# Performance work log

Measured on AMD Instinct MI355X. Metric: run time of the kernel, lower is better.

The kernel has to match this reference:

```python
import jax, jax.numpy as jnp
import numpy as np
import math

B, T, D = 4, 1024, 512
H, HD = 8, 64
FF = 2048
L = 2
MEM = 512
S = T + MEM  # src length
EPS = 1e-5


def _sinusoid(positions, dim):
    pos = positions.astype(jnp.float32)[:, None]                      # [P,1]
    div = jnp.exp(jnp.arange(0, dim, 2, dtype=jnp.float32) * (-math.log(10000.0) / dim))
    enc = jnp.zeros((positions.shape[0], dim), jnp.float32)
    enc = enc.at[:, 0::2].set(jnp.sin(pos * div))
    enc = enc.at[:, 1::2].set(jnp.cos(pos * div))
    return enc


def _layer_norm(x, scale, bias):
    m = jnp.mean(x, axis=-1, keepdims=True)
    v = jnp.var(x, axis=-1, keepdims=True)
    return (x - m) / jnp.sqrt(v + EPS) * scale + bias


def _rel_shift(x):
    # x: [T, S, B, H] -> Transformer-XL relative shift
    t, s, b, h = x.shape
    xp = jnp.concatenate([jnp.zeros((t, 1, b, h), x.dtype), x], axis=1)  # [T,S+1,B,H]
    xp = xp.reshape(s + 1, t, b, h)
    return xp[1:].reshape(t, s, b, h)


def setup_inputs() -> dict:
    key = jax.random.key(0)
    ks = jax.random.split(key, 16)
    w = 0.02
    inp = {
        "x": jax.random.normal(ks[0], (B, T, D), jnp.float32),
        "positions": jnp.arange(S - 1, -1, -1, dtype=jnp.int64 if jax.config.jax_enable_x64 else jnp.int32),
        # causal-with-memory mask: query i (src position i+MEM) cannot see src j > i + MEM
        "attn_mask": jnp.arange(S)[None, :] > (jnp.arange(T)[:, None] + MEM),
        "mems": jax.random.normal(ks[1], (L + 1, MEM, B, D), jnp.float32) * 0.5,
        "u_bias": jax.random.normal(ks[2], (H, HD), jnp.float32) * w,
        "v_bias": jax.random.normal(ks[3], (H, HD), jnp.float32) * w,
        "qkv_w": jax.random.normal(ks[4], (L, 3 * H * HD, D), jnp.float32) * w,
        "pos_w": jax.random.normal(ks[5], (L, H * HD, D), jnp.float32) * w,
        "out_w": jax.random.normal(ks[6], (L, D, H * HD), jnp.float32) * w,
        "lin1_w": jax.random.normal(ks[7], (L, FF, D), jnp.float32) * w,
        "lin1_b": jnp.zeros((L, FF), jnp.float32),
        "lin2_w": jax.random.normal(ks[8], (L, D, FF), jnp.float32) * w,
        "lin2_b": jnp.zeros((L, D), jnp.float32),
        "ln1_s": jnp.ones((L, D), jnp.float32),
        "ln1_b": jnp.zeros((L, D), jnp.float32),
        "ln2_s": jnp.ones((L, D), jnp.float32),
        "ln2_b": jnp.zeros((L, D), jnp.float32),
    }
    return inp


def reference(x, positions, attn_mask, mems, u_bias, v_bias, qkv_w, pos_w, out_w,
              lin1_w, lin1_b, lin2_w, lin2_b, ln1_s, ln1_b, ln2_s, ln2_b):
    scale = 1.0 / math.sqrt(D)  # source uses 1/sqrt(embed_dim)
    xs = jnp.swapaxes(x, 0, 1)                       # [T,B,D] (batch_first -> time-first)
    pe = _sinusoid(positions, D)                     # [S,D]
    out = xs
    hiddens = [xs]
    for l in range(L):
        cat = jnp.concatenate([mems[l], out], axis=0)            # [S,B,D]
        qkv = jnp.einsum('sbd,ed->sbe', cat, qkv_w[l])           # [S,B,3*H*HD]
        q, k, v = jnp.split(qkv, 3, axis=-1)
        q = q[-T:].reshape(T, B, H, HD)
        k = k.reshape(S, B, H, HD)
        v = v.reshape(S, B, H, HD)
        r = jnp.einsum('sd,ed->se', pe, pos_w[l]).reshape(S, H, HD)
        content = jnp.einsum('ibnd,jbnd->ijbn', q + u_bias, k)   # [T,S,B,H]
        pos_sc = jnp.einsum('ibnd,jnd->ijbn', q + v_bias, r)     # [T,S,B,H]
        score = (content + _rel_shift(pos_sc)) * scale
        score = jnp.where(attn_mask[:, :, None, None], -jnp.inf, score)
        attn = jax.nn.softmax(score, axis=1)
        ctx = jnp.einsum('ijbn,jbnd->ibnd', attn, v).reshape(T, B, H * HD)
        a_out = jnp.einsum('tbe,de->tbd', ctx, out_w[l])
        h = _layer_norm(out + a_out, ln1_s[l], ln1_b[l])
        ff = jnp.einsum('tbf,df->tbd', jax.nn.relu(jnp.einsum('tbd,fd->tbf', h, lin1_w[l]) + lin1_b[l]), lin2_w[l]) + lin2_b[l]
        out = _layer_norm(h + ff, ln2_s[l], ln2_b[l])
        hiddens.append(out)
    final = jnp.swapaxes(out[-T:], 0, 1)             # [B,T,D]
    new_mems = jax.lax.stop_gradient(jnp.stack(
        [jnp.concatenate([mems[i], hiddens[i]], axis=0)[-MEM:] for i in range(L + 1)], axis=0))
    return final, new_mems
```

## Files before the change

### kernel.cpp

```cpp
#include <hip/hip_runtime.h>

constexpr int BB = 4, TT = 1024, DD = 512, HH = 8, HDIM = 64;
constexpr int FFD = 2048, NLAYER = 2, MM = 512, SS = 1536;
constexpr float LN_EPS = 1e-5f;
constexpr float SCALE = 0.04419417382415922f;

typedef unsigned short u16;
typedef __attribute__((ext_vector_type(8))) short bf16x8;
typedef __attribute__((ext_vector_type(4))) float f32x4;

__device__ __forceinline__ float b2f(u16 u) {
  union { unsigned int i; float f; } c; c.i = ((unsigned int)u) << 16; return c.f;
}
__device__ __forceinline__ u16 f2b(float f) {
  unsigned int x = __builtin_bit_cast(unsigned int, f);
  x += 0x7fffu + ((x >> 16) & 1u);
  return (u16)(x >> 16);
}

__device__ __forceinline__ void dma16(const u16* g, u16* l) {
  __builtin_amdgcn_global_load_lds(
      (const __attribute__((address_space(1))) unsigned int*)g,
      (__attribute__((address_space(3))) unsigned int*)l, 16, 0, 0);
}

constexpr int OFF_X    = 0;
constexpr int OFF_MEMS = 2097152;
constexpr int OFF_UB   = 5242880;
constexpr int OFF_VB   = 5243392;
constexpr int OFF_QKVW = 5243904;
constexpr int OFF_POSW = 6816768;
constexpr int OFF_OUTW = 7341056;
constexpr int OFF_L1W  = 7865344;
constexpr int OFF_L1B  = 9962496;
constexpr int OFF_L2W  = 9966592;
constexpr int OFF_L2B  = 12063744;
constexpr int OFF_LN1S = 12064768;
constexpr int OFF_LN1B = 12065792;
constexpr int OFF_LN2S = 12066816;
constexpr int OFF_LN2B = 12067840;
constexpr int TOT_IN   = 12068864;

__global__ void txl_probe(const u16* __restrict__ xr, int* __restrict__ flag) {
  int lane = threadIdx.x;
  int cnt = 0;
  for (int k = 0; k < 8; ++k) {
    u16 u = xr[lane * 8 + k];
    int e = (u >> 7) & 0xFF;
    if (e >= 0xC0) ++cnt;
  }
  for (int o = 32; o; o >>= 1) cnt += __shfl_xor(cnt, o);
  if (lane == 0) *flag = (cnt >= 32) ? 1 : 0;
}

__global__ __launch_bounds__(256) void txl_convert(
    const void* x, const void* mems, const void* ub, const void* vb,
    const void* qkvw, const void* posw, const void* outw,
    const void* l1w, const void* l1b, const void* l2w, const void* l2b,
    const void* ln1s, const void* ln1b, const void* ln2s, const void* ln2b,
    u16* __restrict__ dst, const int* __restrict__ flag) {
  int idx = blockIdx.x * 256 + threadIdx.x;
  if (idx >= TOT_IN) return;
  const void* p; int local;
  if      (idx < OFF_MEMS) { p = x;    local = idx; }
  else if (idx < OFF_UB)   { p = mems; local = idx - OFF_MEMS; }
  else if (idx < OFF_VB)   { p = ub;   local = idx - OFF_UB; }
  else if (idx < OFF_QKVW) { p = vb;   local = idx - OFF_VB; }
  else if (idx < OFF_POSW) { p = qkvw; local = idx - OFF_QKVW; }
  else if (idx < OFF_OUTW) { p = posw; local = idx - OFF_POSW; }
  else if (idx < OFF_L1W)  { p = outw; local = idx - OFF_OUTW; }
  else if (idx < OFF_L1B)  { p = l1w;  local = idx - OFF_L1W; }
  else if (idx < OFF_L2W)  { p = l1b;  local = idx - OFF_L1B; }
  else if (idx < OFF_L2B)  { p = l2w;  local = idx - OFF_L2W; }
  else if (idx < OFF_LN1S) { p = l2b;  local = idx - OFF_L2B; }
  else if (idx < OFF_LN1B) { p = ln1s; local = idx - OFF_LN1S; }
  else if (idx < OFF_LN2S) { p = ln1b; local = idx - OFF_LN1B; }
  else if (idx < OFF_LN2B) { p = ln2s; local = idx - OFF_LN2S; }
  else                     { p = ln2b; local = idx - OFF_LN2B; }
  dst[idx] = (*flag) ? f2b(((const float*)p)[local]) : ((const u16*)p)[local];
}

template <int EPI>
__global__ __launch_bounds__(256) void txl_gemm4(const u16* __restrict__ A,
                                                 const u16* __restrict__ B,
                                                 float* __restrict__ C,
                                                 u16* __restrict__ Obf,
                                                 const u16* __restrict__ bias,
                                                 int M, int N, int K, int KS) {
  __shared__ __align__(16) u16 As[2][128 * 32];
  __shared__ __align__(16) u16 Bs[2][128 * 32];
  const int tid = threadIdx.x;
  const int wave = tid >> 6, lane = tid & 63;
  const int wm = (wave & 1) * 64, wn = (wave >> 1) * 64;
  const int m0 = blockIdx.x * 128, n0 = blockIdx.y * 128;
  const int kbeg = blockIdx.z * KS, kend = kbeg + KS;
  const int L15 = lane & 15, quad = lane >> 4;

  auto stage = [&](int k0, int buf) {
    for (int c = 0; c < 2; ++c) {
      int segBase = c * 256 + wave * 64;
      int seg = segBase + lane;
      int row = seg >> 2, q = seg & 3;
      dma16(&A[(size_t)(m0 + row) * K + k0 + q * 8], &As[buf][segBase * 8]);
      dma16(&B[(size_t)(n0 + row) * K + k0 + q * 8], &Bs[buf][segBase * 8]);
    }
  };

  f32x4 acc[4][4] = {};
  stage(kbeg, 0);
  __syncthreads();
  int buf = 0;
  for (int k0 = kbeg; k0 < kend; k0 += 32) {
    if (k0 + 32 < kend) stage(k0 + 32, buf ^ 1);
    bf16x8 af[4], bfr[4];
    for (int t = 0; t < 4; ++t)
      af[t] = *reinterpret_cast<const bf16x8*>(&As[buf][(wm + t * 16 + L15) * 32 + quad * 8]);
    for (int t = 0; t < 4; ++t)
      bfr[t] = *reinterpret_cast<const bf16x8*>(&Bs[buf][(wn + t * 16 + L15) * 32 + quad * 8]);
    for (int tm = 0; tm < 4; ++tm)
      for (int tn = 0; tn < 4; ++tn)
        acc[tm][tn] = __builtin_amdgcn_mfma_f32_16x16x32_bf16(af[tm], bfr[tn], acc[tm][tn], 0, 0, 0);
    buf ^= 1;
    __syncthreads();
  }
  float* Cz = C + (size_t)blockIdx.z * ((size_t)M * N);
  for (int tm = 0; tm < 4; ++tm)
    for (int tn = 0; tn < 4; ++tn) {
      int col = n0 + wn + tn * 16 + L15;
      for (int r = 0; r < 4; ++r) {
        int row = m0 + wm + tm * 16 + quad * 4 + r;
        if (EPI == 0) {
          Cz[(size_t)row * N + col] = acc[tm][tn][r];
        } else {
          float v = acc[tm][tn][r] + b2f(bias[col]);
          Obf[(size_t)row * N + col] = f2b(fmaxf(v, 0.f));
        }
      }
    }
}

__global__ void txl_pe(u16* __restrict__ pe) {
  int idx = blockIdx.x * 256 + threadIdx.x;
  if (idx >= SS * 256) return;
  int p = idx >> 8, m = idx & 255;
  float posf = (float)(SS - 1 - p);
  float div = expf((float)(2 * m) * (-9.210340371976184f / 512.0f));
  float a = posf * div;
  pe[(size_t)p * DD + 2 * m] = f2b(sinf(a));
  pe[(size_t)p * DD + 2 * m + 1] = f2b(cosf(a));
}

__global__ void txl_transpose_in(const u16* __restrict__ x, u16* __restrict__ cur_bf,
                                 float* __restrict__ cur_f, void* __restrict__ outv,
                                 const int* __restrict__ flag) {
  int idx = blockIdx.x * 256 + threadIdx.x;
  if (idx >= BB * TT * DD) return;
  int b = idx >> 19, t = (idx >> 9) & 1023, d = idx & 511;
  u16 v = x[idx];
  size_t o = ((size_t)t * BB + b) * DD + d;
  cur_bf[o] = v; cur_f[o] = b2f(v);
  if (t >= 512) {
    size_t mo = 2097152 + (o - 1048576);
    if (*flag) ((float*)outv)[mo] = b2f(v);
    else       ((u16*)outv)[mo] = v;
  }
}

__global__ void txl_store_final(const u16* __restrict__ cur_bf, void* __restrict__ outv,
                                const int* __restrict__ flag) {
  int idx = blockIdx.x * 256 + threadIdx.x;
  if (idx >= BB * TT * DD) return;
  int b = idx >> 19, t = (idx >> 9) & 1023, d = idx & 511;
  u16 v = cur_bf[((size_t)t * BB + b) * DD + d];
  if (*flag) ((float*)outv)[idx] = b2f(v);
  else       ((u16*)outv)[idx] = v;
}

__global__ __launch_bounds__(256) void txl_qkv_scatter(
    const float* __restrict__ C, const u16* __restrict__ ub, const u16* __restrict__ vb,
    u16* __restrict__ qu, u16* __restrict__ qv, u16* __restrict__ kb) {
  size_t idx = (size_t)blockIdx.x * 256 + threadIdx.x;
  if (idx >= (size_t)SS * BB * 1536) return;
  int e = (int)(idx % 1536);
  if (e >= 1024) return;
  int row = (int)(idx / 1536);
  int s = row >> 2, b = row & 3;
  float val = C[idx];
  if (e < 512) {
    if (s >= MM) {
      int i = s - MM, n = e >> 6, d = e & 63;
      size_t o = ((size_t)(b * HH + n) * TT + i) * HDIM + d;
      qu[o] = f2b(val + b2f(ub[e]));
      qv[o] = f2b(val + b2f(vb[e]));
    }
  } else {
    int e2 = e - 512, n = e2 >> 6, d = e2 & 63;
    kb[((size_t)(b * HH + n) * SS + s) * HDIM + d] = f2b(val);
  }
}

__global__ __launch_bounds__(256) void txl_v_transpose(const float* __restrict__ C,
                                                       u16* __restrict__ vT) {
  __shared__ u16 t[64][68];
  int bx = blockIdx.x;
  int sb = bx >> 5;
  int bn = bx & 31;
  int n = bn & 7, b = bn >> 3;
  int tid = threadIdx.x;
  int s0 = sb * 64;
  {
    int d = tid & 63, sr = tid >> 6;
    for (int i = 0; i < 16; ++i) {
      int s = s0 + sr + i * 4;
      t[sr + i * 4][d] = f2b(C[(size_t)(s * 4 + b) * 1536 + 1024 + n * 64 + d]);
    }
  }
  __syncthreads();
  {
    int s = tid & 63, dr = tid >> 6;
    u16* dst = vT + (size_t)(b * HH + n) * HDIM * SS;
    for (int i = 0; i < 16; ++i) {
      int d2 = dr + i * 4;
      dst[(size_t)d2 * SS + s0 + s] = t[s][d2];
    }
  }
}

__global__ void txl_r_scatter(const float* __restrict__ C, u16* __restrict__ rb) {
  int idx = blockIdx.x * 256 + threadIdx.x;
  if (idx >= SS * DD) return;
  int p = idx >> 9, e = idx & 511;
  int n = e >> 6, d = e & 63;
  rb[((size_t)n * SS + p) * HDIM + d] = f2b(C[idx]);
}

__global__ __launch_bounds__(256) void txl_attn9(
    const u16* __restrict__ qu, const u16* __restrict__ qv, const u16* __restrict__ kbuf,
    const u16* __restrict__ vT, const u16* __restrict__ rbuf,
    float* __restrict__ O0, float* __restrict__ O1,
    float* __restrict__ L0, float* __restrict__ L1) {
  __shared__ __align__(16) u16 Kb[2][2048];
  __shared__ __align__(16) u16 Vb[2][2048];
  __shared__ __align__(16) u16 Rr[8][1024];
  __shared__ __align__(16) u16 ps4[4][640];

  const int bx = blockIdx.x;
  const int n = bx & 7;
  const int rest = bx >> 3;
  const int b = rest & 3;
  const int rest2 = rest >> 2;
  const int st = rest2 & 15;
  const int piece = rest2 >> 4;
  const int i0b = st * 64;
  const int g0 = 63 - (i0b >> 4);
  const int jcEnd = 18 + 2 * st;
  const int half = 9 + st;
  const int jcBeg = piece ? half : 0;
  const int jcLim = piece ? jcEnd : half;
  const int gB = g0 + 2 * jcBeg;

  const int tid = threadIdx.x, w = tid >> 6, lane = tid & 63;
  const int L15 = lane & 15, quad = lane >> 4;
  const int i0w = i0b + 16 * w;
  const int bh = b * HH + n;

  const u16* kB = kbuf + (size_t)bh * SS * HDIM;
  const u16* rB = rbuf + (size_t)n * SS * HDIM;
  const u16* vB = vT + (size_t)bh * HDIM * SS;

  const u16* quB = qu + ((size_t)bh * TT + i0w) * HDIM;
  const u16* qvB = qv + ((size_t)bh * TT + i0w) * HDIM;
  bf16x8 aqu[2], aqv[2];
  for (int c = 0; c < 2; ++c) {
    aqu[c] = *reinterpret_cast<const bf16x8*>(&quB[(size_t)L15 * HDIM + c * 32 + quad * 8]);
    aqv[c] = *reinterpret_cast<const bf16x8*>(&qvB[(size_t)L15 * HDIM + c * 32 + quad * 8]);
  }

  u16* ps = &ps4[w][0];

  auto stageK = [&](int jc) {
    const u16* src = kB + (size_t)(jc * 32 + (lane & 31)) * HDIM + (2 * w + (lane >> 5)) * 8;
    dma16(src, &Kb[jc & 1][512 * w]);
  };
  auto stageV = [&](int jc) {
    const u16* src = vB + (size_t)lane * SS + jc * 32 + 8 * w;
    dma16(src, &Vb[jc & 1][512 * w]);
  };
  auto stageRslab = [&](int slab) {
    int rrow = slab * 16 + (lane & 15);
    rrow = (rrow > SS - 1) ? (SS - 1) : rrow;
    const u16* s0 = rB + (size_t)rrow * HDIM + (lane >> 4) * 8;
    dma16(s0, &Rr[slab & 7][0]);
    dma16(s0 + 32, &Rr[slab & 7][512]);
  };
  auto rfrag = [&](int slab, int h) {
    return *reinterpret_cast<const bf16x8*>(&Rr[slab & 7][((quad + 4 * h) * 16 + L15) * 8]);
  };

  stageK(jcBeg); stageV(jcBeg);
  stageRslab(gB - 3 + w);
  if (w < 2) stageRslab(gB + 1 + w);
  __syncthreads();

  f32x4 pT0 = {};
  pT0 = __builtin_amdgcn_mfma_f32_16x16x32_bf16(aqv[0], rfrag(gB - w, 0), pT0, 0, 0, 0);
  pT0 = __builtin_amdgcn_mfma_f32_16x16x32_bf16(aqv[1], rfrag(gB - w, 1), pT0, 0, 0, 0);

  float l_lane[4] = {0.f, 0.f, 0.f, 0.f};
  f32x4 Oacc[4] = {};

  for (int jc = jcBeg; jc < jcLim; ++jc) {
    if (jc + 1 < jcLim) {
      stageK(jc + 1); stageV(jc + 1);
      if (w < 2) stageRslab(g0 + 3 + 2 * jc + w);
    }
    const int hslot = jc & 1, j0 = jc * 32;
    bf16x8 k00 = *reinterpret_cast<const bf16x8*>(&Kb[hslot][((quad) * 32 + L15) * 8]);
    bf16x8 k01 = *reinterpret_cast<const bf16x8*>(&Kb[hslot][((quad + 4) * 32 + L15) * 8]);
    bf16x8 k10 = *reinterpret_cast<const bf16x8*>(&Kb[hslot][((quad) * 32 + 16 + L15) * 8]);
    bf16x8 k11 = *reinterpret_cast<const bf16x8*>(&Kb[hslot][((quad + 4) * 32 + 16 + L15) * 8]);
    f32x4 s0v = {}, s1v = {};
    s0v = __builtin_amdgcn_mfma_f32_16x16x32_bf16(aqu[0], k00, s0v, 0, 0, 0);
    s0v = __builtin_amdgcn_mfma_f32_16x16x32_bf16(aqu[1], k01, s0v, 0, 0, 0);
    s1v = __builtin_amdgcn_mfma_f32_16x16x32_bf16(aqu[0], k10, s1v, 0, 0, 0);
    s1v = __builtin_amdgcn_mfma_f32_16x16x32_bf16(aqu[1], k11, s1v, 0, 0, 0);
    const int sl1 = g0 - w + 2 * jc + 1;
    f32x4 pT1 = {}, pT2 = {};
    pT1 = __builtin_amdgcn_mfma_f32_16x16x32_bf16(aqv[0], rfrag(sl1, 0), pT1, 0, 0, 0);
    pT1 = __builtin_amdgcn_mfma_f32_16x16x32_bf16(aqv[1], rfrag(sl1, 1), pT1, 0, 0, 0);
    pT2 = __builtin_amdgcn_mfma_f32_16x16x32_bf16(aqv[0], rfrag(sl1 + 1, 0), pT2, 0, 0, 0);
    pT2 = __builtin_amdgcn_mfma_f32_16x16x32_bf16(aqv[1], rfrag(sl1 + 1, 1), pT2, 0, 0, 0);
    for (int r = 0; r < 4; ++r) {
      int ii = quad * 4 + r;
      int i = i0w + ii;
      int c = 15 + L15 - ii;
      int srcLane = (quad << 4) | (c & 15);
      float a0 = __shfl(pT0[r], srcLane);
      float a1 = __shfl(pT1[r], srcLane);
      float b1v = __shfl(pT2[r], srcLane);
      float sv0 = s0v[r] + ((c < 16) ? a0 : a1);
      float sv1 = s1v[r] + ((c < 16) ? a1 : b1v);
      sv0 = (j0 + L15 <= i + MM) ? sv0 : -3e38f;
      sv1 = (j0 + 16 + L15 <= i + MM) ? sv1 : -3e38f;
      float e0 = __expf(sv0 * SCALE);
      float e1 = __expf(sv1 * SCALE);
      l_lane[r] += e0 + e1;
      int row = ii * 40;
      ps[row + L15] = f2b(e0);
      ps[row + 16 + L15] = f2b(e1);
    }
    bf16x8 ap = *reinterpret_cast<const bf16x8*>(&ps[L15 * 40 + quad * 8]);
    bf16x8 v0 = *reinterpret_cast<const bf16x8*>(&Vb[hslot][(quad * 64 + L15) * 8]);
    bf16x8 v1 = *reinterpret_cast<const bf16x8*>(&Vb[hslot][(quad * 64 + 16 + L15) * 8]);
    bf16x8 v2 = *reinterpret_cast<const bf16x8*>(&Vb[hslot][(quad * 64 + 32 + L15) * 8]);
    bf16x8 v3 = *reinterpret_cast<const bf16x8*>(&Vb[hslot][(quad * 64 + 48 + L15) * 8]);
    Oacc[0] = __builtin_amdgcn_mfma_f32_16x16x32_bf16(ap, v0, Oacc[0], 0, 0, 0);
    Oacc[1] = __builtin_amdgcn_mfma_f32_16x16x32_bf16(ap, v1, Oacc[1], 0, 0, 0);
    Oacc[2] = __builtin_amdgcn_mfma_f32_16x16x32_bf16(ap, v2, Oacc[2], 0, 0, 0);
    Oacc[3] = __builtin_amdgcn_mfma_f32_16x16x32_bf16(ap, v3, Oacc[3], 0, 0, 0);
    pT0 = pT2;
    __syncthreads();
  }

  float lsum[4];
  for (int r = 0; r < 4; ++r) {
    float s = l_lane[r];
    for (int o = 1; o < 16; o <<= 1) s += __shfl_xor(s, o);
    lsum[r] = s;
  }
  float* Op = piece ? O1 : O0;
  float* Lp = piece ? L1 : L0;
  for (int tn = 0; tn < 4; ++tn)
    for (int r = 0; r < 4; ++r) {
      int ii = quad * 4 + r;
      Op[((size_t)(i0w + ii) * BB + b) * DD + n * HDIM + tn * 16 + L15] = Oacc[tn][r];
    }
  if (L15 == 0)
    for (int r = 0; r < 4; ++r)
      Lp[(size_t)bh * TT + i0w + quad * 4 + r] = lsum[r];
}

__global__ void txl_attn_merge(const float* __restrict__ O0, const float* __restrict__ O1,
                               const float* __restrict__ L0, const float* __restrict__ L1,
                               u16* __restrict__ ctx) {
  int o = blockIdx.x * 256 + threadIdx.x;
  if (o >= BB * TT * DD) return;
  int i = o >> 11, b = (o >> 9) & 3, e = o & 511, n = e >> 6;
  size_t li = (size_t)(b * HH + n) * TT + i;
  float l = L0[li] + L1[li];
  ctx[o] = f2b((O0[o] + O1[o]) / l);
}

__global__ __launch_bounds__(256) void txl_ln(
    const float* __restrict__ gout, int nparts, const u16* __restrict__ bias,
    const float* __restrict__ resid, const u16* __restrict__ gam, const u16* __restrict__ bet,
    u16* __restrict__ ybf, float* __restrict__ yf,
    void* __restrict__ outv, int off, const int* __restrict__ flag) {
  const int row = blockIdx.x, tid = threadIdx.x;
  const int lane = tid & 63, wave = tid >> 6;
  __shared__ float red[4];
  size_t base = (size_t)row * DD;
  float x0 = resid[base + tid];
  float x1 = resid[base + tid + 256];
  for (int p = 0; p < nparts; ++p) {
    x0 += gout[(size_t)p * 2097152 + base + tid];
    x1 += gout[(size_t)p * 2097152 + base + tid + 256];
  }
  if (bias) { x0 += b2f(bias[tid]); x1 += b2f(bias[tid + 256]); }
  float s = x0 + x1;
  for (int o = 32; o; o >>= 1) s += __shfl_xor(s, o);
  if (lane == 0) red[wave] = s;
  __syncthreads();
  float mean = (red[0] + red[1] + red[2] + red[3]) * (1.f / DD);
  __syncthreads();
  float d0 = x0 - mean, d1 = x1 - mean;
  float q = d0 * d0 + d1 * d1;
  for (int o = 32; o; o >>= 1) q += __shfl_xor(q, o);
  if (lane == 0) red[wave] = q;
  __syncthreads();
  float var = (red[0] + red[1] + red[2] + red[3]) * (1.f / DD);
  float rstd = rsqrtf(var + LN_EPS);
  float y0 = d0 * rstd * b2f(gam[tid]) + b2f(bet[tid]);
  float y1 = d1 * rstd * b2f(gam[tid + 256]) + b2f(bet[tid + 256]);
  u16 u0 = f2b(y0), u1 = f2b(y1);
  ybf[base + tid] = u0;
  ybf[base + tid + 256] = u1;
  yf[base + tid] = y0;
  yf[base + tid + 256] = y1;
  if (outv && row >= 2048) {
    size_t mo = (size_t)off + (size_t)(row - 2048) * DD;
    if (*flag) {
      ((float*)outv)[mo + tid] = y0;
      ((float*)outv)[mo + tid + 256] = y1;
    } else {
      ((u16*)outv)[mo + tid] = u0;
      ((u16*)outv)[mo + tid + 256] = u1;
    }
  }
}

constexpr size_t WS_CUR_F  = 0;
constexpr size_t WS_CAT    = 8388608;
constexpr size_t WS_CBUF   = 14680064;
constexpr size_t WS_QU     = 52428800;
constexpr size_t WS_QV     = 56623104;
constexpr size_t WS_K      = 60817408;
constexpr size_t WS_VT     = 67108864;
constexpr size_t WS_R      = 73400320;
constexpr size_t WS_PE     = 74973184;
constexpr size_t WS_CTX    = 76546048;
constexpr size_t WS_HBF    = 80740352;
constexpr size_t WS_HF     = 84934656;
constexpr size_t WS_FF1    = 93323264;
constexpr size_t WS_CURBF  = 110100480;
constexpr size_t WS_CIN    = 114294784;
constexpr size_t WS_FLAG   = 138432512;
constexpr size_t WS_TOTAL  = 138432576;
constexpr size_t WS_OB0 = WS_CBUF;
constexpr size_t WS_OB1 = WS_CBUF + 8388608;
constexpr size_t WS_LB0 = WS_CBUF + 16777216;
constexpr size_t WS_LB1 = WS_CBUF + 16908288;

extern "C" void kernel_launch(void* const* d_in, const int* in_sizes, int n_in,
                              void* d_out, int out_size, void* d_ws, size_t ws_size,
                              hipStream_t stream) {
  (void)in_sizes; (void)n_in;

  if (ws_size < WS_TOTAL) {
    hipMemsetAsync(d_out, 0, (size_t)out_size * 2, stream);
    return;
  }
  char* ws = (char*)d_ws;
  float* cur_f  = (float*)(ws + WS_CUR_F);
  u16*   cat    = (u16*)(ws + WS_CAT);
  float* Cbuf   = (float*)(ws + WS_CBUF);
  float* Ob0    = (float*)(ws + WS_OB0);
  float* Ob1    = (float*)(ws + WS_OB1);
  float* Lb0    = (float*)(ws + WS_LB0);
  float* Lb1    = (float*)(ws + WS_LB1);
  u16*   qu     = (u16*)(ws + WS_QU);
  u16*   qv     = (u16*)(ws + WS_QV);
  u16*   kb     = (u16*)(ws + WS_K);
  u16*   vT     = (u16*)(ws + WS_VT);
  u16*   rb     = (u16*)(ws + WS_R);
  u16*   pe     = (u16*)(ws + WS_PE);
  u16*   ctx    = (u16*)(ws + WS_CTX);
  u16*   hbf    = (u16*)(ws + WS_HBF);
  float* hf     = (float*)(ws + WS_HF);
  u16*   ff1    = (u16*)(ws + WS_FF1);
  u16*   cur_bf = (u16*)(ws + WS_CURBF);
  u16*   cin    = (u16*)(ws + WS_CIN);
  int*   flag   = (int*)(ws + WS_FLAG);

  txl_probe<<<1, 64, 0, stream>>>((const u16*)d_in[0], flag);
  txl_convert<<<47144, 256, 0, stream>>>(
      d_in[0], d_in[3], d_in[4], d_in[5], d_in[6], d_in[7], d_in[8],
      d_in[9], d_in[10], d_in[11], d_in[12], d_in[13], d_in[14], d_in[15], d_in[16],
      cin, flag);

  const u16* ub = cin + OFF_UB;
  const u16* vb = cin + OFF_VB;

  txl_pe<<<SS, 256, 0, stream>>>(pe);
  txl_transpose_in<<<8192, 256, 0, stream>>>(cin + OFF_X, cur_bf, cur_f, d_out, flag);

  for (int l = 0; l < NLAYER; ++l) {
    hipMemcpyAsync(cat, cin + OFF_MEMS + (size_t)l * 1048576, 2097152,
                   hipMemcpyDeviceToDevice, stream);
    hipMemcpyAsync(cat + 1048576, cur_bf, 4194304, hipMemcpyDeviceToDevice, stream);
    txl_gemm4<0><<<dim3(48, 12, 1), 256, 0, stream>>>(
        cat, cin + OFF_QKVW + (size_t)l * 786432, Cbuf, nullptr, nullptr, 6144, 1536, 512, 512);
    txl_qkv_scatter<<<36864, 256, 0, stream>>>(Cbuf, ub, vb, qu, qv, kb);
    txl_v_transpose<<<768, 256, 0, stream>>>(Cbuf, vT);
    txl_gemm4<0><<<dim3(12, 4, 1), 256, 0, stream>>>(
        pe, cin + OFF_POSW + (size_t)l * 262144, Cbuf, nullptr, nullptr, 1536, 512, 512, 512);
    txl_r_scatter<<<3072, 256, 0, stream>>>(Cbuf, rb);
    txl_attn9<<<1024, 256, 0, stream>>>(qu, qv, kb, vT, rb, Ob0, Ob1, Lb0, Lb1);
    txl_attn_merge<<<8192, 256, 0, stream>>>(Ob0, Ob1, Lb0, Lb1, ctx);
    txl_gemm4<0><<<dim3(32, 4, 2), 256, 0, stream>>>(
        ctx, cin + OFF_OUTW + (size_t)l * 262144, Cbuf, nullptr, nullptr, 4096, 512, 512, 256);
    txl_ln<<<4096, 256, 0, stream>>>(Cbuf, 2, nullptr, cur_f,
                                     cin + OFF_LN1S + l * 512, cin + OFF_LN1B + l * 512,
                                     hbf, hf, nullptr, 0, flag);
    txl_gemm4<1><<<dim3(32, 16, 1), 256, 0, stream>>>(
        hbf, cin + OFF_L1W + (size_t)l * 1048576, nullptr, ff1,
        cin + OFF_L1B + l * 2048, 4096, 2048, 512, 512);
    txl_gemm4<0><<<dim3(32, 4, 4), 256, 0, stream>>>(
        ff1, cin + OFF_L2W + (size_t)l * 1048576, Cbuf, nullptr, nullptr, 4096, 512, 2048, 512);
    txl_ln<<<4096, 256, 0, stream>>>(Cbuf, 4, cin + OFF_L2B + l * 512, hf,
                                     cin + OFF_LN2S + l * 512, cin + OFF_LN2B + l * 512,
                                     cur_bf, cur_f, d_out, 2097152 + (l + 1) * 1048576, flag);
  }
  txl_store_final<<<8192, 256, 0, stream>>>(cur_bf, d_out, flag);
}
```

Before: 496.0 us.

## Fuse small kernels: PE into convert, r-scatter into GEMM, final store into LN

Positional-encoding generation now runs inside the convert kernel's tail blocks. The pos projection GEMM writes bf16 head-major r directly, so the separate scatter kernel is gone. The final output transpose is written by the last layer-norm kernel instead of a separate pass. Attention block-to-query-tile mapping is reversed for the second piece to balance causal work, and epilogue loops are unrolled. Together these cut kernel launches and intermediate fp32 round-trips, at the cost of scattered stores in the new GEMM epilogue.

```diff
diff --git a/kernel.cpp b/kernel.cpp
--- a/kernel.cpp
+++ b/kernel.cpp
@@ -40,6 +40,7 @@
 constexpr int OFF_LN2S = 12066816;
 constexpr int OFF_LN2B = 12067840;
 constexpr int TOT_IN   = 12068864;
+constexpr int PE_CNT   = SS * 256;
 
 __global__ void txl_probe(const u16* __restrict__ xr, int* __restrict__ flag) {
   int lane = threadIdx.x;
@@ -58,9 +59,19 @@
     const void* qkvw, const void* posw, const void* outw,
     const void* l1w, const void* l1b, const void* l2w, const void* l2b,
     const void* ln1s, const void* ln1b, const void* ln2s, const void* ln2b,
-    u16* __restrict__ dst, const int* __restrict__ flag) {
+    u16* __restrict__ dst, u16* __restrict__ pe, const int* __restrict__ flag) {
   int idx = blockIdx.x * 256 + threadIdx.x;
-  if (idx >= TOT_IN) return;
+  if (idx >= TOT_IN) {
+    int idx2 = idx - TOT_IN;
+    if (idx2 >= PE_CNT) return;
+    int p = idx2 >> 8, m = idx2 & 255;
+    float posf = (float)(SS - 1 - p);
+    float div = expf((float)(2 * m) * (-9.210340371976184f / 512.0f));
+    float a = posf * div;
+    pe[(size_t)p * DD + 2 * m] = f2b(sinf(a));
+    pe[(size_t)p * DD + 2 * m + 1] = f2b(cosf(a));
+    return;
+  }
   const void* p; int local;
   if      (idx < OFF_MEMS) { p = x;    local = idx; }
   else if (idx < OFF_UB)   { p = mems; local = idx - OFF_MEMS; }
@@ -124,9 +135,12 @@
     __syncthreads();
   }
   float* Cz = C + (size_t)blockIdx.z * ((size_t)M * N);
+#pragma unroll
   for (int tm = 0; tm < 4; ++tm)
+#pragma unroll
     for (int tn = 0; tn < 4; ++tn) {
       int col = n0 + wn + tn * 16 + L15;
+#pragma unroll
       for (int r = 0; r < 4; ++r) {
         int row = m0 + wm + tm * 16 + quad * 4 + r;
         if (EPI == 0) {
@@ -139,15 +153,57 @@
     }
 }
 
-__global__ void txl_pe(u16* __restrict__ pe) {
-  int idx = blockIdx.x * 256 + threadIdx.x;
-  if (idx >= SS * 256) return;
-  int p = idx >> 8, m = idx & 255;
-  float posf = (float)(SS - 1 - p);
-  float div = expf((float)(2 * m) * (-9.210340371976184f / 512.0f));
-  float a = posf * div;
-  pe[(size_t)p * DD + 2 * m] = f2b(sinf(a));
-  pe[(size_t)p * DD + 2 * m + 1] = f2b(cosf(a));
+__global__ __launch_bounds__(256) void txl_gemm_r(const u16* __restrict__ A,
+                                                  const u16* __restrict__ B,
+                                                  u16* __restrict__ rb,
+                                                  int M, int N, int K) {
+  __shared__ __align__(16) u16 As[2][128 * 32];
+  __shared__ __align__(16) u16 Bs[2][128 * 32];
+  const int tid = threadIdx.x;
+  const int wave = tid >> 6, lane = tid & 63;
+  const int wm = (wave & 1) * 64, wn = (wave >> 1) * 64;
+  const int m0 = blockIdx.x * 128, n0 = blockIdx.y * 128;
+  const int L15 = lane & 15, quad = lane >> 4;
+
+  auto stage = [&](int k0, int buf) {
+    for (int c = 0; c < 2; ++c) {
+      int segBase = c * 256 + wave * 64;
+      int seg = segBase + lane;
+      int row = seg >> 2, q = seg & 3;
+      dma16(&A[(size_t)(m0 + row) * K + k0 + q * 8], &As[buf][segBase * 8]);
+      dma16(&B[(size_t)(n0 + row) * K + k0 + q * 8], &Bs[buf][segBase * 8]);
+    }
+  };
+
+  f32x4 acc[4][4] = {};
+  stage(0, 0);
+  __syncthreads();
+  int buf = 0;
+  for (int k0 = 0; k0 < K; k0 += 32) {
+    if (k0 + 32 < K) stage(k0 + 32, buf ^ 1);
+    bf16x8 af[4], bfr[4];
+    for (int t = 0; t < 4; ++t)
+      af[t] = *reinterpret_cast<const bf16x8*>(&As[buf][(wm + t * 16 + L15) * 32 + quad * 8]);
+    for (int t = 0; t < 4; ++t)
+      bfr[t] = *reinterpret_cast<const bf16x8*>(&Bs[buf][(wn + t * 16 + L15) * 32 + quad * 8]);
+    for (int tm = 0; tm < 4; ++tm)
+      for (int tn = 0; tn < 4; ++tn)
+        acc[tm][tn] = __builtin_amdgcn_mfma_f32_16x16x32_bf16(af[tm], bfr[tn], acc[tm][tn], 0, 0, 0);
+    buf ^= 1;
+    __syncthreads();
+  }
+#pragma unroll
+  for (int tm = 0; tm < 4; ++tm)
+#pragma unroll
+    for (int tn = 0; tn < 4; ++tn) {
+      int col = n0 + wn + tn * 16 + L15;
+      int n = col >> 6, d = col & 63;
+#pragma unroll
+      for (int r = 0; r < 4; ++r) {
+        int row = m0 + wm + tm * 16 + quad * 4 + r;
+        rb[((size_t)n * SS + row) * HDIM + d] = f2b(acc[tm][tn][r]);
+      }
+    }
 }
 
 __global__ void txl_transpose_in(const u16* __restrict__ x, u16* __restrict__ cur_bf,
@@ -164,16 +220,6 @@
     if (*flag) ((float*)outv)[mo] = b2f(v);
     else       ((u16*)outv)[mo] = v;
   }
-}
-
-__global__ void txl_store_final(const u16* __restrict__ cur_bf, void* __restrict__ outv,
-                                const int* __restrict__ flag) {
-  int idx = blockIdx.x * 256 + threadIdx.x;
-  if (idx >= BB * TT * DD) return;
-  int b = idx >> 19, t = (idx >> 9) & 1023, d = idx & 511;
-  u16 v = cur_bf[((size_t)t * BB + b) * DD + d];
-  if (*flag) ((float*)outv)[idx] = b2f(v);
-  else       ((u16*)outv)[idx] = v;
 }
 
 __global__ __launch_bounds__(256) void txl_qkv_scatter(
@@ -226,14 +272,6 @@
   }
 }
 
-__global__ void txl_r_scatter(const float* __restrict__ C, u16* __restrict__ rb) {
-  int idx = blockIdx.x * 256 + threadIdx.x;
-  if (idx >= SS * DD) return;
-  int p = idx >> 9, e = idx & 511;
-  int n = e >> 6, d = e & 63;
-  rb[((size_t)n * SS + p) * HDIM + d] = f2b(C[idx]);
-}
-
 __global__ __launch_bounds__(256) void txl_attn9(
     const u16* __restrict__ qu, const u16* __restrict__ qv, const u16* __restrict__ kbuf,
     const u16* __restrict__ vT, const u16* __restrict__ rbuf,
@@ -249,8 +287,8 @@
   const int rest = bx >> 3;
   const int b = rest & 3;
   const int rest2 = rest >> 2;
-  const int st = rest2 & 15;
   const int piece = rest2 >> 4;
+  const int st = piece ? (15 - (rest2 & 15)) : (rest2 & 15);
   const int i0b = st * 64;
   const int g0 = 63 - (i0b >> 4);
   const int jcEnd = 18 + 2 * st;
@@ -395,7 +433,8 @@
     const float* __restrict__ gout, int nparts, const u16* __restrict__ bias,
     const float* __restrict__ resid, const u16* __restrict__ gam, const u16* __restrict__ bet,
     u16* __restrict__ ybf, float* __restrict__ yf,
-    void* __restrict__ outv, int off, const int* __restrict__ flag) {
+    void* __restrict__ outv, int off, void* __restrict__ finalv,
+    const int* __restrict__ flag) {
   const int row = blockIdx.x, tid = threadIdx.x;
   const int lane = tid & 63, wave = tid >> 6;
   __shared__ float red[4];
@@ -435,6 +474,17 @@
     } else {
       ((u16*)outv)[mo + tid] = u0;
       ((u16*)outv)[mo + tid + 256] = u1;
+    }
+  }
+  if (finalv) {
+    int t = row >> 2, b = row & 3;
+    size_t fo = ((size_t)b * TT + t) * DD;
+    if (*flag) {
+      ((float*)finalv)[fo + tid] = y0;
+      ((float*)finalv)[fo + tid + 256] = y1;
+    } else {
+      ((u16*)finalv)[fo + tid] = u0;
+      ((u16*)finalv)[fo + tid + 256] = u1;
     }
   }
 }
@@ -493,15 +543,14 @@
   int*   flag   = (int*)(ws + WS_FLAG);
 
   txl_probe<<<1, 64, 0, stream>>>((const u16*)d_in[0], flag);
-  txl_convert<<<47144, 256, 0, stream>>>(
+  txl_convert<<<48680, 256, 0, stream>>>(
       d_in[0], d_in[3], d_in[4], d_in[5], d_in[6], d_in[7], d_in[8],
       d_in[9], d_in[10], d_in[11], d_in[12], d_in[13], d_in[14], d_in[15], d_in[16],
-      cin, flag);
+      cin, pe, flag);
 
   const u16* ub = cin + OFF_UB;
   const u16* vb = cin + OFF_VB;
 
-  txl_pe<<<SS, 256, 0, stream>>>(pe);
   txl_transpose_in<<<8192, 256, 0, stream>>>(cin + OFF_X, cur_bf, cur_f, d_out, flag);
 
   for (int l = 0; l < NLAYER; ++l) {
@@ -512,16 +561,15 @@
         cat, cin + OFF_QKVW + (size_t)l * 786432, Cbuf, nullptr, nullptr, 6144, 1536, 512, 512);
     txl_qkv_scatter<<<36864, 256, 0, stream>>>(Cbuf, ub, vb, qu, qv, kb);
     txl_v_transpose<<<768, 256, 0, stream>>>(Cbuf, vT);
-    txl_gemm4<0><<<dim3(12, 4, 1), 256, 0, stream>>>(
-        pe, cin + OFF_POSW + (size_t)l * 262144, Cbuf, nullptr, nullptr, 1536, 512, 512, 512);
-    txl_r_scatter<<<3072, 256, 0, stream>>>(Cbuf, rb);
+    txl_gemm_r<<<dim3(12, 4), 256, 0, stream>>>(
+        pe, cin + OFF_POSW + (size_t)l * 262144, rb, 1536, 512, 512);
     txl_attn9<<<1024, 256, 0, stream>>>(qu, qv, kb, vT, rb, Ob0, Ob1, Lb0, Lb1);
     txl_attn_merge<<<8192, 256, 0, stream>>>(Ob0, Ob1, Lb0, Lb1, ctx);
     txl_gemm4<0><<<dim3(32, 4, 2), 256, 0, stream>>>(
         ctx, cin + OFF_OUTW + (size_t)l * 262144, Cbuf, nullptr, nullptr, 4096, 512, 512, 256);
     txl_ln<<<4096, 256, 0, stream>>>(Cbuf, 2, nullptr, cur_f,
                                      cin + OFF_LN1S + l * 512, cin + OFF_LN1B + l * 512,
-                                     hbf, hf, nullptr, 0, flag);
+                                     hbf, hf, nullptr, 0, nullptr, flag);
     txl_gemm4<1><<<dim3(32, 16, 1), 256, 0, stream>>>(
         hbf, cin + OFF_L1W + (size_t)l * 1048576, nullptr, ff1,
         cin + OFF_L1B + l * 2048, 4096, 2048, 512, 512);
@@ -529,7 +577,7 @@
         ff1, cin + OFF_L2W + (size_t)l * 1048576, Cbuf, nullptr, nullptr, 4096, 512, 2048, 512);
     txl_ln<<<4096, 256, 0, stream>>>(Cbuf, 4, cin + OFF_L2B + l * 512, hf,
                                      cin + OFF_LN2S + l * 512, cin + OFF_LN2B + l * 512,
-                                     cur_bf, cur_f, d_out, 2097152 + (l + 1) * 1048576, flag);
-  }
-  txl_store_final<<<8192, 256, 0, stream>>>(cur_bf, d_out, flag);
-}
+                                     cur_bf, cur_f, d_out, 2097152 + (l + 1) * 1048576,
+                                     (l == NLAYER - 1) ? d_out : nullptr, flag);
+  }
+}
```

Measured after the change: 476.0 us. 1.04x faster.
